# Kernel optimization log

Hardware: AMD Instinct MI355X
Metric: run time of the kernel (lower is better)

Reference implementation:

```python
import jax, jax.numpy as jnp
import numpy as np

B, N, HD, U = 2, 512, 64, 128  # batch, nodes, h_dim, mlp width


def _init(key, shape):
    return jax.random.normal(key, shape, dtype=jnp.float32) / np.sqrt(shape[0]).astype(np.float32)


def setup_inputs() -> dict:
    key = jax.random.key(0)
    ks = jax.random.split(key, 12)
    x = jax.random.normal(ks[0], (B, N, 3), dtype=jnp.float32)
    h = jax.random.normal(ks[1], (B, N, HD), dtype=jnp.float32)
    p = {}
    p['We1'] = _init(ks[2], (1 + 2 * HD, U)); p['be1'] = jnp.zeros((U,), jnp.float32)
    p['We2'] = _init(ks[3], (U, U));          p['be2'] = jnp.zeros((U,), jnp.float32)
    p['Winf'] = _init(ks[4], (U, 1));         p['binf'] = jnp.zeros((1,), jnp.float32)
    p['Wx1'] = _init(ks[5], (U, U));          p['bx1'] = jnp.zeros((U,), jnp.float32)
    p['Wx2'] = _init(ks[6], (U, U));          p['bx2'] = jnp.zeros((U,), jnp.float32)
    p['Wx3'] = _init(ks[7], (U, 1));          p['bx3'] = jnp.zeros((1,), jnp.float32)
    p['Wh1'] = _init(ks[8], (U + HD, U));     p['bh1'] = jnp.zeros((U,), jnp.float32)
    p['Wh2'] = _init(ks[9], (U, U));          p['bh2'] = jnp.zeros((U,), jnp.float32)
    p['Wout'] = _init(ks[10], (U, HD));       p['bout'] = jnp.zeros((HD,), jnp.float32)
    return {'x': x, 'h': h, **p}


def _mlp2(t, W1, b1, W2, b2):
    # hk.nets.MLP([U, U], activation=elu), activate_final=False
    return jax.nn.elu(t @ W1 + b1) @ W2 + b2


def reference(x, h, We1, be1, We2, be2, Winf, binf, Wx1, bx1, Wx2, bx2, Wx3, bx3, Wh1, bh1, Wh2, bh2, Wout, bout):
    Bn, Nn, _ = x.shape
    hd = h.shape[-1]
    mask = 1.0 - jnp.eye(Nn, dtype=x.dtype)  # zero the i==j diagonal
    # diff[b,i,j] = x[b,j] - x[b,i]  (matches x - x[:, None] in the original)
    diff = (x[:, None, :, :] - x[:, :, None, :]) * mask[None, :, :, None]  # [B,N,N,3]
    sq = jnp.sum(diff * diff, axis=-1)
    norms = jnp.sqrt(jnp.where(mask > 0, sq, 1.0)) * mask  # safe sqrt; diag exactly 0
    # h_combos[b,i,j] = concat(h[b,j], h[b,i])
    h_j = jnp.broadcast_to(h[:, None, :, :], (Bn, Nn, Nn, hd))
    h_i = jnp.broadcast_to(h[:, :, None, :], (Bn, Nn, Nn, hd))
    feat = jnp.concatenate([norms[..., None], h_j, h_i], axis=-1)  # [B,N,N,1+2*hd]
    m_ij = _mlp2(feat, We1, be1, We2, be2) * mask[None, :, :, None]  # [B,N,N,U]
    e = jax.nn.sigmoid(m_ij @ Winf + binf)[..., 0] * mask            # [B,N,N]
    m_i = jnp.einsum('bijd,bij->bid', m_ij, e)                       # [B,N,U]
    # phi_x: MLP(activate_final=True) then Linear(1)
    hid = jax.nn.elu(jax.nn.elu(m_ij @ Wx1 + bx1) @ Wx2 + bx2)
    phi_x_out = (hid @ Wx3 + bx3)[..., 0] * mask                     # [B,N,N]
    shift = jnp.einsum('bijd,bij->bid', diff, phi_x_out) / (Nn - 1)  # [B,N,3]
    h_new = _mlp2(jnp.concatenate([m_i, h], axis=-1), Wh1, bh1, Wh2, bh2) @ Wout + bout
    return (x + shift, h_new)
```

## Files before the change

kernel.cpp:

```cpp
#include <hip/hip_runtime.h>
#include <math.h>


#define BB    2
#define NN    512
#define HDIM  64
#define UDIM  128
#define JT    32
#define NTILE (NN / JT)
#define FP    72
#define PP    136

typedef float f32x4 __attribute__((ext_vector_type(4)));
typedef short s16x8 __attribute__((ext_vector_type(8)));

__device__ __forceinline__ ushort f2bf(float f) {
    union { float f; unsigned u; } v; v.f = f;
    return (ushort)((v.u + 0x7FFFu + ((v.u >> 16) & 1u)) >> 16);
}
__device__ __forceinline__ float bf2f(ushort s) {
    union { unsigned u; float f; } v; v.u = ((unsigned)s) << 16; return v.f;
}
__device__ __forceinline__ f32x4 MFMA(s16x8 a, s16x8 b, f32x4 c) {
    return __builtin_amdgcn_mfma_f32_16x16x32_bf16(a, b, c, 0, 0, 0);
}
__device__ __forceinline__ float eluf(float v) { return v > 0.f ? v : __expf(v) - 1.f; }

__device__ __forceinline__ void load_wfrags(const float* __restrict__ W, int q, int ucol,
                                            s16x8 (&dst)[4][2]) {
#pragma unroll
    for (int s = 0; s < 4; ++s)
#pragma unroll
        for (int n = 0; n < 2; ++n) {
            s16x8 r;
#pragma unroll
            for (int ii = 0; ii < 8; ++ii)
                r[ii] = (short)f2bf(W[(32 * s + 8 * q + ii) * UDIM + ucol + 16 * n]);
            dst[s][n] = r;
        }
}

template <int KSTEPS, int PITCH>
__device__ __forceinline__ void gemm_P(const ushort* __restrict__ P, const s16x8 (&wB)[KSTEPS][2],
                                       int l15, int q, f32x4 (&acc)[2][2]) {
#pragma unroll
    for (int s = 0; s < KSTEPS; ++s) {
        const s16x8 a0 = *(const s16x8*)(P + l15 * PITCH + 32 * s + 8 * q);
        const s16x8 a1 = *(const s16x8*)(P + (16 + l15) * PITCH + 32 * s + 8 * q);
        acc[0][0] = MFMA(a0, wB[s][0], acc[0][0]);
        acc[0][1] = MFMA(a0, wB[s][1], acc[0][1]);
        acc[1][0] = MFMA(a1, wB[s][0], acc[1][0]);
        acc[1][1] = MFMA(a1, wB[s][1], acc[1][1]);
    }
}

template <bool ELU>
__device__ __forceinline__ void store_P(ushort* __restrict__ P, const f32x4 (&v)[2][2],
                                        int q, int uc0, int uc1) {
#pragma unroll
    for (int m = 0; m < 2; ++m)
#pragma unroll
        for (int r = 0; r < 4; ++r) {
            const int row = 16 * m + 4 * q + r;
            float a = v[m][0][r], c = v[m][1][r];
            if (ELU) { a = eluf(a); c = eluf(c); }
            P[row * PP + uc0] = f2bf(a);
            P[row * PP + uc1] = f2bf(c);
        }
}

__global__ __launch_bounds__(256, 2) void egnn_mfma(
    const float* __restrict__ x, const float* __restrict__ h,
    const float* __restrict__ We1, const float* __restrict__ be1,
    const float* __restrict__ We2, const float* __restrict__ be2,
    const float* __restrict__ Winf, const float* __restrict__ binf,
    const float* __restrict__ Wx1, const float* __restrict__ bx1,
    const float* __restrict__ Wx2, const float* __restrict__ bx2,
    const float* __restrict__ Wx3, const float* __restrict__ bx3,
    const float* __restrict__ Wh1, const float* __restrict__ bh1,
    const float* __restrict__ Wh2, const float* __restrict__ bh2,
    const float* __restrict__ Wout, const float* __restrict__ bout,
    float* __restrict__ out) {
    __shared__ ushort F[JT][FP];
    __shared__ ushort P1[JT][PP];
    __shared__ ushort P2[JT][PP];
    __shared__ float normL[JT];
    __shared__ float diffL[JT][3];
    __shared__ float rpart[8][JT];
    __shared__ float eL[JT];
    __shared__ float bias1L[UDIM];
    __shared__ float WinfL[UDIM], Wx3L[UDIM];
    __shared__ float catL[UDIM + HDIM];
    __shared__ float th1[UDIM], th2[UDIM];

    const int bi = blockIdx.x;
    const int b  = bi >> 9;
    const int i  = bi & (NN - 1);
    const int tid  = threadIdx.x;
    const int lane = tid & 63;
    const int w    = tid >> 6;
    const int l15  = lane & 15;
    const int q    = lane >> 4;
    const int uc0  = 32 * w + l15, uc1 = uc0 + 16;

    s16x8 wB1[2][2];
#pragma unroll
    for (int s = 0; s < 2; ++s)
#pragma unroll
        for (int n = 0; n < 2; ++n) {
            s16x8 r;
#pragma unroll
            for (int ii = 0; ii < 8; ++ii)
                r[ii] = (short)f2bf(We1[(1 + 32 * s + 8 * q + ii) * UDIM + uc0 + 16 * n]);
            wB1[s][n] = r;
        }
    s16x8 wB2[4][2], wB3[4][2], wB4[4][2];
    load_wfrags(We2, q, uc0, wB2);
    load_wfrags(Wx1, q, uc0, wB3);
    load_wfrags(Wx2, q, uc0, wB4);

    if (tid < UDIM) {
        WinfL[tid] = Winf[tid];
        Wx3L[tid]  = Wx3[tid];
        float s = be1[tid];
        const float* hi = &h[(b * NN + i) * HDIM];
#pragma unroll 8
        for (int k = 0; k < HDIM; ++k)
            s = fmaf(hi[k], We1[(1 + HDIM + k) * UDIM + tid], s);
        bias1L[tid] = s;
    }
    const float w0n0 = We1[uc0], w0n1 = We1[uc1];
    const float b2n0 = be2[uc0], b2n1 = be2[uc1];
    const float bqn0 = bx1[uc0], bqn1 = bx1[uc1];
    const float brn0 = bx2[uc0], brn1 = bx2[uc1];
    const float binf0 = binf[0], bx30 = bx3[0];
    const float xi0 = x[(b * NN + i) * 3 + 0];
    const float xi1 = x[(b * NN + i) * 3 + 1];
    const float xi2 = x[(b * NN + i) * 3 + 2];
    __syncthreads();
    const float b1n0 = bias1L[uc0], b1n1 = bias1L[uc1];

    float mi0 = 0.f, mi1 = 0.f;
    float sh0 = 0.f, sh1 = 0.f, sh2 = 0.f;

    for (int t = 0; t < NTILE; ++t) {
        const int j0 = t * JT;
        __syncthreads();

        {
            const int j = tid >> 3, k0 = (tid & 7) * 8;
            const float* hp = &h[(b * NN + j0 + j) * HDIM + k0];
            const float4 f0 = *(const float4*)hp;
            const float4 f1 = *(const float4*)(hp + 4);
            s16x8 r;
            r[0] = (short)f2bf(f0.x); r[1] = (short)f2bf(f0.y);
            r[2] = (short)f2bf(f0.z); r[3] = (short)f2bf(f0.w);
            r[4] = (short)f2bf(f1.x); r[5] = (short)f2bf(f1.y);
            r[6] = (short)f2bf(f1.z); r[7] = (short)f2bf(f1.w);
            *(s16x8*)&F[j][k0] = r;
        }
        if (tid < JT) {
            const int j = j0 + tid;
            float d0 = x[(b * NN + j) * 3 + 0] - xi0;
            float d1 = x[(b * NN + j) * 3 + 1] - xi1;
            float d2 = x[(b * NN + j) * 3 + 2] - xi2;
            if (j == i) { d0 = 0.f; d1 = 0.f; d2 = 0.f; }
            diffL[tid][0] = d0; diffL[tid][1] = d1; diffL[tid][2] = d2;
            normL[tid] = (j == i) ? 0.f : sqrtf(d0 * d0 + d1 * d1 + d2 * d2);
        }
        __syncthreads();

        float nrm[2][4];
#pragma unroll
        for (int m = 0; m < 2; ++m)
#pragma unroll
            for (int r = 0; r < 4; ++r) nrm[m][r] = normL[16 * m + 4 * q + r];
        f32x4 acc[2][2];
#pragma unroll
        for (int m = 0; m < 2; ++m)
#pragma unroll
            for (int r = 0; r < 4; ++r) {
                acc[m][0][r] = fmaf(nrm[m][r], w0n0, b1n0);
                acc[m][1][r] = fmaf(nrm[m][r], w0n1, b1n1);
            }
        gemm_P<2, FP>(&F[0][0], wB1, l15, q, acc);
        store_P<true>(&P1[0][0], acc, q, uc0, uc1);
        __syncthreads();

        f32x4 macc[2][2];
#pragma unroll
        for (int m = 0; m < 2; ++m)
#pragma unroll
            for (int r = 0; r < 4; ++r) { macc[m][0][r] = b2n0; macc[m][1][r] = b2n1; }
        gemm_P<4, PP>(&P1[0][0], wB2, l15, q, macc);
#pragma unroll
        for (int m = 0; m < 2; ++m)
#pragma unroll
            for (int r = 0; r < 4; ++r)
                if (j0 + 16 * m + 4 * q + r == i) { macc[m][0][r] = 0.f; macc[m][1][r] = 0.f; }
        store_P<false>(&P2[0][0], macc, q, uc0, uc1);
        __syncthreads();

        {
            const int j = tid & 31, uch = tid >> 5, u0 = uch * 16;
            const s16x8 m0 = *(const s16x8*)&P2[j][u0];
            const s16x8 m1 = *(const s16x8*)&P2[j][u0 + 8];
            float p = 0.f;
#pragma unroll
            for (int c = 0; c < 8; ++c) p = fmaf(bf2f((ushort)m0[c]), WinfL[u0 + c], p);
#pragma unroll
            for (int c = 0; c < 8; ++c) p = fmaf(bf2f((ushort)m1[c]), WinfL[u0 + 8 + c], p);
            rpart[uch][j] = p;
        }
        f32x4 qacc[2][2];
#pragma unroll
        for (int m = 0; m < 2; ++m)
#pragma unroll
            for (int r = 0; r < 4; ++r) { qacc[m][0][r] = bqn0; qacc[m][1][r] = bqn1; }
        gemm_P<4, PP>(&P2[0][0], wB3, l15, q, qacc);
        store_P<true>(&P1[0][0], qacc, q, uc0, uc1);
        __syncthreads();

        if (tid < 32) {
            float s = 0.f;
#pragma unroll
            for (int p = 0; p < 8; ++p) s += rpart[p][tid];
            float e = 1.f / (1.f + __expf(-(s + binf0)));
            if (j0 + tid == i) e = 0.f;
            eL[tid] = e;
        }
        f32x4 racc[2][2];
#pragma unroll
        for (int m = 0; m < 2; ++m)
#pragma unroll
            for (int r = 0; r < 4; ++r) { racc[m][0][r] = brn0; racc[m][1][r] = brn1; }
        gemm_P<4, PP>(&P1[0][0], wB4, l15, q, racc);
        store_P<true>(&P2[0][0], racc, q, uc0, uc1);
        __syncthreads();

        {
            const int j = tid & 31, uch = tid >> 5, u0 = uch * 16;
            const s16x8 m0 = *(const s16x8*)&P2[j][u0];
            const s16x8 m1 = *(const s16x8*)&P2[j][u0 + 8];
            float p = 0.f;
#pragma unroll
            for (int c = 0; c < 8; ++c) p = fmaf(bf2f((ushort)m0[c]), Wx3L[u0 + c], p);
#pragma unroll
            for (int c = 0; c < 8; ++c) p = fmaf(bf2f((ushort)m1[c]), Wx3L[u0 + 8 + c], p);
            rpart[uch][j] = p;
        }
        {
            float el[2][4];
#pragma unroll
            for (int m = 0; m < 2; ++m)
#pragma unroll
                for (int r = 0; r < 4; ++r) el[m][r] = eL[16 * m + 4 * q + r];
#pragma unroll
            for (int m = 0; m < 2; ++m)
#pragma unroll
                for (int r = 0; r < 4; ++r) {
                    mi0 = fmaf(macc[m][0][r], el[m][r], mi0);
                    mi1 = fmaf(macc[m][1][r], el[m][r], mi1);
                }
        }
        __syncthreads();

        if (tid < 64) {
            const int l = tid & 31;
            float s = 0.f;
#pragma unroll
            for (int p = 0; p < 8; ++p) s += rpart[p][l];
            s += bx30;
            if (j0 + l == i) s = 0.f;
            float v0 = 0.f, v1 = 0.f, v2 = 0.f;
            if (tid < 32) {
                v0 = diffL[l][0] * s; v1 = diffL[l][1] * s; v2 = diffL[l][2] * s;
            }
#pragma unroll
            for (int d = 1; d < 64; d <<= 1) {
                v0 += __shfl_xor(v0, d);
                v1 += __shfl_xor(v1, d);
                v2 += __shfl_xor(v2, d);
            }
            sh0 += v0; sh1 += v1; sh2 += v2;
        }
    }

    __syncthreads();
    {
        float v0 = mi0, v1 = mi1;
        v0 += __shfl_xor(v0, 16); v0 += __shfl_xor(v0, 32);
        v1 += __shfl_xor(v1, 16); v1 += __shfl_xor(v1, 32);
        if (lane < 16) {
            catL[32 * w + lane]      = v0;
            catL[32 * w + 16 + lane] = v1;
        }
    }
    if (tid >= 128 && tid < 128 + HDIM)
        catL[UDIM + tid - 128] = h[(b * NN + i) * HDIM + (tid - 128)];
    if (tid == 0) {
        const float inv = 1.f / (float)(NN - 1);
        out[(b * NN + i) * 3 + 0] = x[(b * NN + i) * 3 + 0] + sh0 * inv;
        out[(b * NN + i) * 3 + 1] = x[(b * NN + i) * 3 + 1] + sh1 * inv;
        out[(b * NN + i) * 3 + 2] = x[(b * NN + i) * 3 + 2] + sh2 * inv;
    }
    __syncthreads();

    if (tid < UDIM) {
        float s = bh1[tid];
        for (int k = 0; k < UDIM + HDIM; ++k) s = fmaf(catL[k], Wh1[k * UDIM + tid], s);
        th1[tid] = eluf(s);
    }
    __syncthreads();
    if (tid < UDIM) {
        float s = bh2[tid];
        for (int k = 0; k < UDIM; ++k) s = fmaf(th1[k], Wh2[k * UDIM + tid], s);
        th2[tid] = s;
    }
    __syncthreads();
    if (tid < HDIM) {
        float s = bout[tid];
        for (int k = 0; k < UDIM; ++k) s = fmaf(th2[k], Wout[k * HDIM + tid], s);
        out[BB * NN * 3 + (b * NN + i) * HDIM + tid] = s;
    }
}

extern "C" void kernel_launch(void* const* d_in, const int* in_sizes, int n_in,
                              void* d_out, int out_size, void* d_ws, size_t ws_size,
                              hipStream_t stream) {
    const float* x    = (const float*)d_in[0];
    const float* h    = (const float*)d_in[1];
    const float* We1  = (const float*)d_in[2];
    const float* be1  = (const float*)d_in[3];
    const float* We2  = (const float*)d_in[4];
    const float* be2  = (const float*)d_in[5];
    const float* Winf = (const float*)d_in[6];
    const float* binf = (const float*)d_in[7];
    const float* Wx1  = (const float*)d_in[8];
    const float* bx1  = (const float*)d_in[9];
    const float* Wx2  = (const float*)d_in[10];
    const float* bx2  = (const float*)d_in[11];
    const float* Wx3  = (const float*)d_in[12];
    const float* bx3  = (const float*)d_in[13];
    const float* Wh1  = (const float*)d_in[14];
    const float* bh1  = (const float*)d_in[15];
    const float* Wh2  = (const float*)d_in[16];
    const float* bh2  = (const float*)d_in[17];
    const float* Wout = (const float*)d_in[18];
    const float* bout = (const float*)d_in[19];
    float* out = (float*)d_out;

    hipLaunchKernelGGL(egnn_mfma, dim3(BB * NN), dim3(256), 0, stream,
                       x, h, We1, be1, We2, be2, Winf, binf, Wx1, bx1, Wx2, bx2,
                       Wx3, bx3, Wh1, bh1, Wh2, bh2, Wout, bout, out);
}
```

Measured before the change: 158.9 us.

## Interleave MFMA output columns, pack bf16 stores, raise occupancy to 4 blocks

Each lane now owns two adjacent output columns instead of columns 16 apart, so pairs of results are converted with v_cvt_pk_bf16_f32 and written as one 32-bit LDS store. Input h tiles are also converted using the packed instruction instead of manual rounding. Launch bounds rise from 2 to 4 blocks per SIMD, which squeezes registers holding roughly 56 weight fragments and may cause spills. Rounding behaviour may differ slightly from the manual f2bf.

```diff
diff --git a/kernel.cpp b/kernel.cpp
--- a/kernel.cpp
+++ b/kernel.cpp
@@ -21,12 +21,17 @@
 __device__ __forceinline__ float bf2f(ushort s) {
     union { unsigned u; float f; } v; v.u = ((unsigned)s) << 16; return v.f;
 }
+__device__ __forceinline__ unsigned pk2(float lo, float hi) {
+    unsigned r;
+    asm("v_cvt_pk_bf16_f32 %0, %1, %2" : "=v"(r) : "v"(lo), "v"(hi));
+    return r;
+}
 __device__ __forceinline__ f32x4 MFMA(s16x8 a, s16x8 b, f32x4 c) {
     return __builtin_amdgcn_mfma_f32_16x16x32_bf16(a, b, c, 0, 0, 0);
 }
 __device__ __forceinline__ float eluf(float v) { return v > 0.f ? v : __expf(v) - 1.f; }
 
-__device__ __forceinline__ void load_wfrags(const float* __restrict__ W, int q, int ucol,
+__device__ __forceinline__ void load_wfrags(const float* __restrict__ W, int q, int uc0,
                                             s16x8 (&dst)[4][2]) {
 #pragma unroll
     for (int s = 0; s < 4; ++s)
@@ -35,7 +40,7 @@
             s16x8 r;
 #pragma unroll
             for (int ii = 0; ii < 8; ++ii)
-                r[ii] = (short)f2bf(W[(32 * s + 8 * q + ii) * UDIM + ucol + 16 * n]);
+                r[ii] = (short)f2bf(W[(32 * s + 8 * q + ii) * UDIM + uc0 + n]);
             dst[s][n] = r;
         }
 }
@@ -56,7 +61,7 @@
 
 template <bool ELU>
 __device__ __forceinline__ void store_P(ushort* __restrict__ P, const f32x4 (&v)[2][2],
-                                        int q, int uc0, int uc1) {
+                                        int q, int uc0) {
 #pragma unroll
     for (int m = 0; m < 2; ++m)
 #pragma unroll
@@ -64,12 +69,11 @@
             const int row = 16 * m + 4 * q + r;
             float a = v[m][0][r], c = v[m][1][r];
             if (ELU) { a = eluf(a); c = eluf(c); }
-            P[row * PP + uc0] = f2bf(a);
-            P[row * PP + uc1] = f2bf(c);
-        }
-}
-
-__global__ __launch_bounds__(256, 2) void egnn_mfma(
+            *(unsigned*)(P + row * PP + uc0) = pk2(a, c);
+        }
+}
+
+__global__ __launch_bounds__(256, 4) void egnn_mfma(
     const float* __restrict__ x, const float* __restrict__ h,
     const float* __restrict__ We1, const float* __restrict__ be1,
     const float* __restrict__ We2, const float* __restrict__ be2,
@@ -101,7 +105,7 @@
     const int w    = tid >> 6;
     const int l15  = lane & 15;
     const int q    = lane >> 4;
-    const int uc0  = 32 * w + l15, uc1 = uc0 + 16;
+    const int uc0  = 32 * w + 2 * l15;
 
     s16x8 wB1[2][2];
 #pragma unroll
@@ -111,7 +115,7 @@
             s16x8 r;
 #pragma unroll
             for (int ii = 0; ii < 8; ++ii)
-                r[ii] = (short)f2bf(We1[(1 + 32 * s + 8 * q + ii) * UDIM + uc0 + 16 * n]);
+                r[ii] = (short)f2bf(We1[(1 + 32 * s + 8 * q + ii) * UDIM + uc0 + n]);
             wB1[s][n] = r;
         }
     s16x8 wB2[4][2], wB3[4][2], wB4[4][2];
@@ -129,16 +133,16 @@
             s = fmaf(hi[k], We1[(1 + HDIM + k) * UDIM + tid], s);
         bias1L[tid] = s;
     }
-    const float w0n0 = We1[uc0], w0n1 = We1[uc1];
-    const float b2n0 = be2[uc0], b2n1 = be2[uc1];
-    const float bqn0 = bx1[uc0], bqn1 = bx1[uc1];
-    const float brn0 = bx2[uc0], brn1 = bx2[uc1];
+    const float w0n0 = We1[uc0], w0n1 = We1[uc0 + 1];
+    const float b2n0 = be2[uc0], b2n1 = be2[uc0 + 1];
+    const float bqn0 = bx1[uc0], bqn1 = bx1[uc0 + 1];
+    const float brn0 = bx2[uc0], brn1 = bx2[uc0 + 1];
     const float binf0 = binf[0], bx30 = bx3[0];
     const float xi0 = x[(b * NN + i) * 3 + 0];
     const float xi1 = x[(b * NN + i) * 3 + 1];
     const float xi2 = x[(b * NN + i) * 3 + 2];
     __syncthreads();
-    const float b1n0 = bias1L[uc0], b1n1 = bias1L[uc1];
+    const float b1n0 = bias1L[uc0], b1n1 = bias1L[uc0 + 1];
 
     float mi0 = 0.f, mi1 = 0.f;
     float sh0 = 0.f, sh1 = 0.f, sh2 = 0.f;
@@ -152,12 +156,10 @@
             const float* hp = &h[(b * NN + j0 + j) * HDIM + k0];
             const float4 f0 = *(const float4*)hp;
             const float4 f1 = *(const float4*)(hp + 4);
-            s16x8 r;
-            r[0] = (short)f2bf(f0.x); r[1] = (short)f2bf(f0.y);
-            r[2] = (short)f2bf(f0.z); r[3] = (short)f2bf(f0.w);
-            r[4] = (short)f2bf(f1.x); r[5] = (short)f2bf(f1.y);
-            r[6] = (short)f2bf(f1.z); r[7] = (short)f2bf(f1.w);
-            *(s16x8*)&F[j][k0] = r;
+            uint4 pv;
+            pv.x = pk2(f0.x, f0.y); pv.y = pk2(f0.z, f0.w);
+            pv.z = pk2(f1.x, f1.y); pv.w = pk2(f1.z, f1.w);
+            *(uint4*)&F[j][k0] = pv;
         }
         if (tid < JT) {
             const int j = j0 + tid;
@@ -170,21 +172,17 @@
         }
         __syncthreads();
 
-        float nrm[2][4];
-#pragma unroll
-        for (int m = 0; m < 2; ++m)
-#pragma unroll
-            for (int r = 0; r < 4; ++r) nrm[m][r] = normL[16 * m + 4 * q + r];
         f32x4 acc[2][2];
 #pragma unroll
         for (int m = 0; m < 2; ++m)
 #pragma unroll
             for (int r = 0; r < 4; ++r) {
-                acc[m][0][r] = fmaf(nrm[m][r], w0n0, b1n0);
-                acc[m][1][r] = fmaf(nrm[m][r], w0n1, b1n1);
+                const float nrm = normL[16 * m + 4 * q + r];
+                acc[m][0][r] = fmaf(nrm, w0n0, b1n0);
+                acc[m][1][r] = fmaf(nrm, w0n1, b1n1);
             }
         gemm_P<2, FP>(&F[0][0], wB1, l15, q, acc);
-        store_P<true>(&P1[0][0], acc, q, uc0, uc1);
+        store_P<true>(&P1[0][0], acc, q, uc0);
         __syncthreads();
 
         f32x4 macc[2][2];
@@ -198,7 +196,7 @@
 #pragma unroll
             for (int r = 0; r < 4; ++r)
                 if (j0 + 16 * m + 4 * q + r == i) { macc[m][0][r] = 0.f; macc[m][1][r] = 0.f; }
-        store_P<false>(&P2[0][0], macc, q, uc0, uc1);
+        store_P<false>(&P2[0][0], macc, q, uc0);
         __syncthreads();
 
         {
@@ -218,7 +216,7 @@
 #pragma unroll
             for (int r = 0; r < 4; ++r) { qacc[m][0][r] = bqn0; qacc[m][1][r] = bqn1; }
         gemm_P<4, PP>(&P2[0][0], wB3, l15, q, qacc);
-        store_P<true>(&P1[0][0], qacc, q, uc0, uc1);
+        store_P<true>(&P1[0][0], qacc, q, uc0);
         __syncthreads();
 
         if (tid < 32) {
@@ -235,7 +233,7 @@
 #pragma unroll
             for (int r = 0; r < 4; ++r) { racc[m][0][r] = brn0; racc[m][1][r] = brn1; }
         gemm_P<4, PP>(&P1[0][0], wB4, l15, q, racc);
-        store_P<true>(&P2[0][0], racc, q, uc0, uc1);
+        store_P<true>(&P2[0][0], racc, q, uc0);
         __syncthreads();
 
         {
@@ -249,20 +247,14 @@
             for (int c = 0; c < 8; ++c) p = fmaf(bf2f((ushort)m1[c]), Wx3L[u0 + 8 + c], p);
             rpart[uch][j] = p;
         }
-        {
-            float el[2][4];
-#pragma unroll
-            for (int m = 0; m < 2; ++m)
-#pragma unroll
-                for (int r = 0; r < 4; ++r) el[m][r] = eL[16 * m + 4 * q + r];
-#pragma unroll
-            for (int m = 0; m < 2; ++m)
-#pragma unroll
-                for (int r = 0; r < 4; ++r) {
-                    mi0 = fmaf(macc[m][0][r], el[m][r], mi0);
-                    mi1 = fmaf(macc[m][1][r], el[m][r], mi1);
-                }
-        }
+#pragma unroll
+        for (int m = 0; m < 2; ++m)
+#pragma unroll
+            for (int r = 0; r < 4; ++r) {
+                const float e = eL[16 * m + 4 * q + r];
+                mi0 = fmaf(macc[m][0][r], e, mi0);
+                mi1 = fmaf(macc[m][1][r], e, mi1);
+            }
         __syncthreads();
 
         if (tid < 64) {
@@ -292,8 +284,8 @@
         v0 += __shfl_xor(v0, 16); v0 += __shfl_xor(v0, 32);
         v1 += __shfl_xor(v1, 16); v1 += __shfl_xor(v1, 32);
         if (lane < 16) {
-            catL[32 * w + lane]      = v0;
-            catL[32 * w + 16 + lane] = v1;
+            catL[uc0]     = v0;
+            catL[uc0 + 1] = v1;
         }
     }
     if (tid >= 128 && tid < 128 + HDIM)
```

New measurement: 441.0 us. +177.5%, slower.
